# Kernel optimization log

Measured on AMD Instinct MI355X. Metric: run time of the kernel, lower is better.

## Reference

```python
import jax, jax.numpy as jnp
import numpy as np

SM_STEPS = 10

def setup_inputs() -> dict:
    key = jax.random.key(0)
    k0, k1, k2, k3 = jax.random.split(key, 4)
    B, N, D, A = 8, 2048, 512, 128
    X = jax.random.normal(k0, (B, N, D), jnp.float32)
    adj = jax.random.uniform(k1, (B, N, N), jnp.float32)
    adj = adj / jnp.sum(adj, axis=-1, keepdims=True)  # row-stochastic for stable diffusion
    mask = jnp.ones((B, N), jnp.float32)
    W1 = jax.random.normal(k2, (A, D), jnp.float32) / np.sqrt(D).astype(np.float32)
    b1 = jnp.zeros((A,), jnp.float32)
    w2 = jax.random.normal(k3, (1, A), jnp.float32) / np.sqrt(A).astype(np.float32)
    alpha_logit = jnp.zeros((), jnp.float32)  # trainable alpha = sigmoid(0) = 0.5
    return {"X": X, "adj": adj, "mask": mask, "W1": W1, "b1": b1, "w2": w2, "alpha_logit": alpha_logit}

def _sm(f, adj, alpha, num_steps):
    # approx Sm: g <- alpha * adj @ g + (1 - alpha) * f, iterated num_steps times
    def body(g, _):
        g = alpha * jnp.einsum('bij,bjd->bid', adj, g) + (1.0 - alpha) * f
        return g, None
    g, _ = jax.lax.scan(body, f, None, length=num_steps)
    return g

def reference(X, adj, mask, W1, b1, w2, alpha_logit):
    alpha = jax.nn.sigmoid(alpha_logit)
    Xs = _sm(X, adj, alpha, SM_STEPS)                     # sm_where == 'early'
    H = jnp.einsum('bnd,ad->bna', Xs, W1) + b1            # proj1: (B,N,att_dim)
    H = jax.nn.gelu(H, approximate=False)                 # torch gelu (erf)
    f = jnp.einsum('bna,oa->bno', H, w2)                  # proj2: (B,N,1)
    m = mask[..., None]                                   # (B,N,1)
    logits = jnp.where(m > 0, f, -jnp.inf)
    s = jax.nn.softmax(logits, axis=1)                    # masked softmax over bag dim
    z = jnp.einsum('bnd,bno->bd', Xs, s)                  # bmm(X^T, s).squeeze(-1)
    return z
```

## Files before the change

### kernel.cpp

```cpp
#include <hip/hip_runtime.h>

constexpr int BB = 8;
constexpr int NN = 2048;
constexpr int DD = 512;
constexpr int AA = 128;
constexpr int SM_STEPS = 10;

typedef __attribute__((ext_vector_type(8))) short bf16x8;
typedef __attribute__((ext_vector_type(4))) float f32x4;
typedef __attribute__((ext_vector_type(8))) unsigned short u16x8;

__device__ __forceinline__ float bf2f(unsigned short u) {
  unsigned int v = ((unsigned int)u) << 16;
  union { unsigned int i; float f; } c; c.i = v; return c.f;
}
__device__ __forceinline__ unsigned short f2bf(float f) {
  union { float f; unsigned int i; } c; c.f = f;
  unsigned int v = c.i;
  unsigned int r = (v + 0x7FFFu + ((v >> 16) & 1u)) >> 16;
  return (unsigned short)r;
}

#define GLOBAL_AS __attribute__((address_space(1)))
#define LDS_AS __attribute__((address_space(3)))

__device__ __forceinline__ void async16(const void* g, void* l) {
  __builtin_amdgcn_global_load_lds((GLOBAL_AS const void*)g, (LDS_AS void*)l, 16, 0, 0);
}

__global__ __launch_bounds__(256) void convert_adj_kernel(
    const float* __restrict__ adj, unsigned short* __restrict__ adjb) {
  size_t i = (size_t)blockIdx.x * blockDim.x + threadIdx.x;
  size_t total = (size_t)BB * NN * NN / 4;
  size_t stride = (size_t)gridDim.x * blockDim.x;
  for (; i < total; i += stride) {
    float4 v = ((const float4*)adj)[i];
    ushort4 o;
    o.x = f2bf(v.x); o.y = f2bf(v.y); o.z = f2bf(v.z); o.w = f2bf(v.w);
    ((ushort4*)adjb)[i] = o;
  }
}

__global__ __launch_bounds__(256) void convert_w1_kernel(
    const float* __restrict__ W1, unsigned short* __restrict__ w1b) {
  int i = blockIdx.x * 256 + threadIdx.x;
  float4 v = ((const float4*)W1)[i];
  ushort4 o;
  o.x = f2bf(v.x); o.y = f2bf(v.y); o.z = f2bf(v.z); o.w = f2bf(v.w);
  ((ushort4*)w1b)[i] = o;
}

__global__ __launch_bounds__(256) void transpose_x_kernel(
    const float* __restrict__ X, unsigned short* __restrict__ xt) {
  __shared__ float tile[64][65];
  const int b = blockIdx.z;
  const int n0 = blockIdx.x * 64, d0 = blockIdx.y * 64;
  const int t = threadIdx.x;
  for (int i = 0; i < 16; ++i) {
    int idx = t + i * 256;
    int r = idx >> 6, c = idx & 63;
    tile[r][c] = X[(size_t)b * NN * DD + (size_t)(n0 + r) * DD + d0 + c];
  }
  __syncthreads();
  for (int i = 0; i < 16; ++i) {
    int idx = t + i * 256;
    int r = idx >> 6, c = idx & 63;
    xt[(size_t)b * DD * NN + (size_t)(d0 + r) * NN + n0 + c] = f2bf(tile[c][r]);
  }
}

__global__ __launch_bounds__(256) void transpose_xs_kernel(
    const unsigned short* __restrict__ xst, unsigned short* __restrict__ gnorm) {
  __shared__ unsigned int tile[64][65];
  const int b = blockIdx.z;
  const int n0 = blockIdx.x * 64, d0 = blockIdx.y * 64;
  const int t = threadIdx.x;
  for (int i = 0; i < 16; ++i) {
    int idx = t + i * 256;
    int r = idx >> 6, c = idx & 63;
    tile[r][c] = xst[(size_t)b * DD * NN + (size_t)(d0 + r) * NN + n0 + c];
  }
  __syncthreads();
  for (int i = 0; i < 16; ++i) {
    int idx = t + i * 256;
    int r = idx >> 6, c = idx & 63;
    gnorm[(size_t)b * NN * DD + (size_t)(n0 + r) * DD + d0 + c] =
        (unsigned short)tile[c][r];
  }
}

__global__ __launch_bounds__(256) void sm_step_kernel(
    const unsigned short* __restrict__ adjb,
    const unsigned short* __restrict__ gin,
    const unsigned short* __restrict__ xt,
    unsigned short* __restrict__ gout,
    const float* __restrict__ alogit) {
  constexpr int BK = 64;
  __shared__ alignas(16) unsigned short As[128 * BK];
  __shared__ alignas(16) unsigned short Bs[128 * BK];

  const int t = threadIdx.x;
  const int b = blockIdx.z;
  const int m0 = blockIdx.y * 128;
  const int n0 = blockIdx.x * 128;

  const int lane = t & 63;
  const int wave = t >> 6;
  const int wr = wave >> 1, wc = wave & 1;
  const int ln = lane & 15, kq = lane >> 4;

  const unsigned short* gA =
      gin + (size_t)b * DD * NN + (size_t)(m0 + (t >> 3)) * NN + (t & 7) * 8;
  const unsigned short* gB =
      adjb + (size_t)b * NN * NN + (size_t)(n0 + (t >> 3)) * NN + (t & 7) * 8;

  f32x4 acc[4][4];
#pragma unroll
  for (int i = 0; i < 4; ++i)
#pragma unroll
    for (int j = 0; j < 4; ++j) acc[i][j] = {0.f, 0.f, 0.f, 0.f};

  for (int k0 = 0; k0 < NN; k0 += BK) {
#pragma unroll
    for (int c = 0; c < 4; ++c) {
      async16(gA + (size_t)(32 * c) * NN, As + 8 * t + 2048 * c);
      async16(gB + (size_t)(32 * c) * NN, Bs + 8 * t + 2048 * c);
    }
    gA += BK;
    gB += BK;
    asm volatile("s_waitcnt vmcnt(0)" ::: "memory");
    __syncthreads();

#pragma unroll
    for (int s = 0; s < 2; ++s) {
      bf16x8 af[4], bfr[4];
#pragma unroll
      for (int i = 0; i < 4; ++i)
        af[i] = *(const bf16x8*)(&As[(wr * 64 + i * 16 + ln) * BK + s * 32 + kq * 8]);
#pragma unroll
      for (int j = 0; j < 4; ++j)
        bfr[j] = *(const bf16x8*)(&Bs[(wc * 64 + j * 16 + ln) * BK + s * 32 + kq * 8]);
#pragma unroll
      for (int i = 0; i < 4; ++i)
#pragma unroll
        for (int j = 0; j < 4; ++j)
          acc[i][j] =
              __builtin_amdgcn_mfma_f32_16x16x32_bf16(af[i], bfr[j], acc[i][j], 0, 0, 0);
    }
    __syncthreads();
  }

  const float al = alogit[0];
  const float alpha = 1.0f / (1.0f + expf(-al));
  const float ia = 1.0f - alpha;

#pragma unroll
  for (int i = 0; i < 4; ++i) {
#pragma unroll
    for (int j = 0; j < 4; ++j) {
      const int mbase = m0 + wr * 64 + i * 16 + kq * 4;
      const int nn = n0 + wc * 64 + j * 16 + ln;
#pragma unroll
      for (int r = 0; r < 4; ++r) {
        size_t idx = (size_t)b * DD * NN + (size_t)(mbase + r) * NN + nn;
        float xv = bf2f(xt[idx]);
        gout[idx] = f2bf(alpha * acc[i][j][r] + ia * xv);
      }
    }
  }
}

__global__ __launch_bounds__(256) void proj_gemm_kernel(
    const unsigned short* __restrict__ gnorm,
    const unsigned short* __restrict__ w1b,
    const float* __restrict__ b1,
    const float* __restrict__ w2,
    float* __restrict__ fbuf) {
  constexpr int BK = 64;
  __shared__ alignas(16) unsigned short As[128 * BK];
  __shared__ alignas(16) unsigned short Bs[128 * BK];
  __shared__ float red[4][64];

  const int t = threadIdx.x;
  const int b = blockIdx.y;
  const int n0 = blockIdx.x * 128;

  const int lane = t & 63;
  const int wave = t >> 6;
  const int wr = wave >> 1, wc = wave & 1;
  const int ln = lane & 15, kq = lane >> 4;

  const unsigned short* gA =
      gnorm + (size_t)b * NN * DD + (size_t)(n0 + (t >> 3)) * DD + (t & 7) * 8;
  const unsigned short* gB = w1b + (size_t)(t >> 3) * DD + (t & 7) * 8;

  f32x4 acc[4][4];
#pragma unroll
  for (int i = 0; i < 4; ++i)
#pragma unroll
    for (int j = 0; j < 4; ++j) acc[i][j] = {0.f, 0.f, 0.f, 0.f};

  for (int k0 = 0; k0 < DD; k0 += BK) {
#pragma unroll
    for (int c = 0; c < 4; ++c) {
      async16(gA + (size_t)(32 * c) * DD, As + 8 * t + 2048 * c);
      async16(gB + (size_t)(32 * c) * DD, Bs + 8 * t + 2048 * c);
    }
    gA += BK;
    gB += BK;
    asm volatile("s_waitcnt vmcnt(0)" ::: "memory");
    __syncthreads();

#pragma unroll
    for (int s = 0; s < 2; ++s) {
      bf16x8 af[4], bfr[4];
#pragma unroll
      for (int i = 0; i < 4; ++i)
        af[i] = *(const bf16x8*)(&As[(wr * 64 + i * 16 + ln) * BK + s * 32 + kq * 8]);
#pragma unroll
      for (int j = 0; j < 4; ++j)
        bfr[j] = *(const bf16x8*)(&Bs[(wc * 64 + j * 16 + ln) * BK + s * 32 + kq * 8]);
#pragma unroll
      for (int i = 0; i < 4; ++i)
#pragma unroll
        for (int j = 0; j < 4; ++j)
          acc[i][j] =
              __builtin_amdgcn_mfma_f32_16x16x32_bf16(af[i], bfr[j], acc[i][j], 0, 0, 0);
    }
    __syncthreads();
  }

  float b1v[4], w2v[4];
#pragma unroll
  for (int j = 0; j < 4; ++j) {
    int a = wc * 64 + j * 16 + ln;
    b1v[j] = b1[a];
    w2v[j] = w2[a];
  }
  float p[4][4];
#pragma unroll
  for (int i = 0; i < 4; ++i)
#pragma unroll
    for (int r = 0; r < 4; ++r) {
      float s = 0.f;
#pragma unroll
      for (int j = 0; j < 4; ++j) {
        float x = acc[i][j][r] + b1v[j];
        float g = 0.5f * x * (1.0f + erff(x * 0.70710678118654752f));
        s += g * w2v[j];
      }
      p[i][r] = s;
    }
#pragma unroll
  for (int m = 1; m < 16; m <<= 1)
#pragma unroll
    for (int i = 0; i < 4; ++i)
#pragma unroll
      for (int r = 0; r < 4; ++r) p[i][r] += __shfl_xor(p[i][r], m);

  if (ln == 0) {
#pragma unroll
    for (int i = 0; i < 4; ++i)
#pragma unroll
      for (int r = 0; r < 4; ++r) red[wave][i * 16 + kq * 4 + r] = p[i][r];
  }
  __syncthreads();
  if (t < 128) {
    int w0 = (t >> 6) * 2, loc = t & 63;
    fbuf[(size_t)b * NN + n0 + t] = red[w0][loc] + red[w0 + 1][loc];
  }
}

__global__ __launch_bounds__(256) void softmax_kernel(
    const float* __restrict__ fbuf, const float* __restrict__ mask,
    float* __restrict__ sbuf) {
  __shared__ float red[8];
  const int b = blockIdx.x, t = threadIdx.x;
  float v[8];
  float mx = -INFINITY;
  for (int i = 0; i < 8; ++i) {
    int n = t + i * 256;
    float mk = mask[(size_t)b * NN + n];
    float lv = fbuf[(size_t)b * NN + n];
    v[i] = (mk > 0.f) ? lv : -INFINITY;
    mx = fmaxf(mx, v[i]);
  }
  for (int d = 32; d; d >>= 1) mx = fmaxf(mx, __shfl_xor(mx, d));
  if ((t & 63) == 0) red[t >> 6] = mx;
  __syncthreads();
  mx = fmaxf(fmaxf(red[0], red[1]), fmaxf(red[2], red[3]));
  float sum = 0.f;
  float e[8];
  for (int i = 0; i < 8; ++i) {
    e[i] = (v[i] == -INFINITY) ? 0.f : expf(v[i] - mx);
    sum += e[i];
  }
  for (int d = 32; d; d >>= 1) sum += __shfl_xor(sum, d);
  if ((t & 63) == 0) red[4 + (t >> 6)] = sum;
  __syncthreads();
  sum = red[4] + red[5] + red[6] + red[7];
  float inv = 1.0f / sum;
  for (int i = 0; i < 8; ++i) sbuf[(size_t)b * NN + t + i * 256] = e[i] * inv;
}

__global__ __launch_bounds__(256) void pool_kernel(
    const unsigned short* __restrict__ xst, const float* __restrict__ sbuf,
    float* __restrict__ zout) {
  __shared__ float sL[NN];
  const int b = blockIdx.y, t = threadIdx.x;
  const int d0 = blockIdx.x * 8;
  for (int i = 0; i < 8; ++i) sL[t + i * 256] = sbuf[(size_t)b * NN + t + i * 256];
  __syncthreads();
  const int row = t >> 5, c = t & 31;
  const int d = d0 + row;
  const unsigned short* xr = xst + (size_t)b * DD * NN + (size_t)d * NN;
  float acc = 0.f;
  for (int i = 0; i < 8; ++i) {
    int nb = c * 64 + i * 8;
    u16x8 x = *(const u16x8*)(xr + nb);
#pragma unroll
    for (int j = 0; j < 8; ++j) acc += bf2f((unsigned short)x[j]) * sL[nb + j];
  }
  for (int dlt = 16; dlt; dlt >>= 1) acc += __shfl_xor(acc, dlt);
  if (c == 0) zout[(size_t)b * DD + d] = acc;
}

extern "C" void kernel_launch(void* const* d_in, const int* in_sizes, int n_in,
                              void* d_out, int out_size, void* d_ws, size_t ws_size,
                              hipStream_t stream) {
  const float* X = (const float*)d_in[0];
  const float* adj = (const float*)d_in[1];
  const float* mask = (const float*)d_in[2];
  const float* W1 = (const float*)d_in[3];
  const float* b1 = (const float*)d_in[4];
  const float* w2 = (const float*)d_in[5];
  const float* alogit = (const float*)d_in[6];
  float* zout = (float*)d_out;

  char* ws = (char*)d_ws;
  unsigned short* adjb = (unsigned short*)ws;
  unsigned short* w1b = (unsigned short*)ws;
  unsigned short* xt = (unsigned short*)(ws + ((size_t)64 << 20));
  unsigned short* gnorm = (unsigned short*)(ws + ((size_t)64 << 20));
  unsigned short* p0 = (unsigned short*)(ws + ((size_t)80 << 20));
  unsigned short* p1 = (unsigned short*)(ws + ((size_t)96 << 20));
  float* fbuf = (float*)(ws + ((size_t)112 << 20));
  float* sbuf = (float*)(ws + ((size_t)112 << 20) + 65536);

  hipLaunchKernelGGL(convert_adj_kernel, dim3(2048), dim3(256), 0, stream, adj, adjb);
  hipLaunchKernelGGL(transpose_x_kernel, dim3(32, 8, 8), dim3(256), 0, stream, X, xt);

  const unsigned short* gin = xt;
  unsigned short* pp[2] = {p0, p1};
  for (int s = 0; s < SM_STEPS; ++s) {
    unsigned short* go = pp[s & 1];
    hipLaunchKernelGGL(sm_step_kernel, dim3(16, 4, 8), dim3(256), 0, stream, adjb, gin,
                       xt, go, alogit);
    gin = go;
  }

  hipLaunchKernelGGL(convert_w1_kernel, dim3(64), dim3(256), 0, stream, W1, w1b);
  hipLaunchKernelGGL(transpose_xs_kernel, dim3(32, 8, 8), dim3(256), 0, stream, gin,
                     gnorm);
  hipLaunchKernelGGL(proj_gemm_kernel, dim3(16, 8), dim3(256), 0, stream, gnorm, w1b,
                     b1, w2, fbuf);
  hipLaunchKernelGGL(softmax_kernel, dim3(8), dim3(256), 0, stream, fbuf, mask, sbuf);
  hipLaunchKernelGGL(pool_kernel, dim3(64, 8), dim3(256), 0, stream, gin, sbuf, zout);
}
```

Baseline: 587.6 us.

## Triple-buffer the diffusion GEMM with swizzled LDS and wider 128x256 tiles

The smoothing-step GEMM now loads tiles into a three-slot LDS ring buffer with async copies issued two K-steps ahead, replacing the old load-wait-compute loop that fully drained memory on every step. Each block grows to 512 threads covering a 128x256 output tile, which halves the grid and reuses each gin tile across more adj columns. LDS addresses are XOR-swizzled to avoid bank conflicts, and s_setprio is raised around the MFMA bursts. The cost is much more LDS per block (about 144 KB), which limits how many blocks fit per CU, and fewer blocks in total.

```diff
diff --git a/kernel.cpp b/kernel.cpp
--- a/kernel.cpp
+++ b/kernel.cpp
@@ -89,30 +89,58 @@
   }
 }
 
-__global__ __launch_bounds__(256) void sm_step_kernel(
+__global__ __launch_bounds__(512) void sm_step_kernel(
     const unsigned short* __restrict__ adjb,
     const unsigned short* __restrict__ gin,
     const unsigned short* __restrict__ xt,
     unsigned short* __restrict__ gout,
     const float* __restrict__ alogit) {
   constexpr int BK = 64;
-  __shared__ alignas(16) unsigned short As[128 * BK];
-  __shared__ alignas(16) unsigned short Bs[128 * BK];
+  __shared__ alignas(16) unsigned char Abuf[3][128 * BK * 2];
+  __shared__ alignas(16) unsigned char Bbuf[3][256 * BK * 2];
 
   const int t = threadIdx.x;
   const int b = blockIdx.z;
   const int m0 = blockIdx.y * 128;
-  const int n0 = blockIdx.x * 128;
+  const int n0 = blockIdx.x * 256;
 
   const int lane = t & 63;
   const int wave = t >> 6;
-  const int wr = wave >> 1, wc = wave & 1;
+  const int wr = wave >> 2;
+  const int wc = wave & 3;
   const int ln = lane & 15, kq = lane >> 4;
 
-  const unsigned short* gA =
-      gin + (size_t)b * DD * NN + (size_t)(m0 + (t >> 3)) * NN + (t & 7) * 8;
-  const unsigned short* gB =
-      adjb + (size_t)b * NN * NN + (size_t)(n0 + (t >> 3)) * NN + (t & 7) * 8;
+  const unsigned short* gA = gin + (size_t)b * DD * NN;
+  const unsigned short* gB = adjb + (size_t)b * NN * NN;
+  const unsigned short* aSrc[2];
+  const unsigned short* bSrc[4];
+  int aOff[2], bOff[4];
+#pragma unroll
+  for (int u = 0; u < 2; ++u) {
+    int o = u * 8192 + t * 16;
+    int q = o ^ (((o >> 7) & 7) << 4);
+    int row = q >> 7, colb = q & 127;
+    aSrc[u] = gA + (size_t)(m0 + row) * NN + colb / 2;
+    aOff[u] = o;
+  }
+#pragma unroll
+  for (int u = 0; u < 4; ++u) {
+    int o = u * 8192 + t * 16;
+    int q = o ^ (((o >> 7) & 7) << 4);
+    int row = q >> 7, colb = q & 127;
+    bSrc[u] = gB + (size_t)(n0 + row) * NN + colb / 2;
+    bOff[u] = o;
+  }
+
+#define STAGE(tkv)                                            \
+  do {                                                        \
+    const int sl_ = (tkv) % 3;                                \
+    const int kk_ = (tkv)*BK;                                 \
+    _Pragma("unroll") for (int u = 0; u < 2; ++u)             \
+        async16(aSrc[u] + kk_, &Abuf[sl_][aOff[u]]);          \
+    _Pragma("unroll") for (int u = 0; u < 4; ++u)             \
+        async16(bSrc[u] + kk_, &Bbuf[sl_][bOff[u]]);          \
+  } while (0)
 
   f32x4 acc[4][4];
 #pragma unroll
@@ -120,35 +148,55 @@
 #pragma unroll
     for (int j = 0; j < 4; ++j) acc[i][j] = {0.f, 0.f, 0.f, 0.f};
 
-  for (int k0 = 0; k0 < NN; k0 += BK) {
-#pragma unroll
-    for (int c = 0; c < 4; ++c) {
-      async16(gA + (size_t)(32 * c) * NN, As + 8 * t + 2048 * c);
-      async16(gB + (size_t)(32 * c) * NN, Bs + 8 * t + 2048 * c);
-    }
-    gA += BK;
-    gB += BK;
-    asm volatile("s_waitcnt vmcnt(0)" ::: "memory");
-    __syncthreads();
-
-#pragma unroll
-    for (int s = 0; s < 2; ++s) {
-      bf16x8 af[4], bfr[4];
-#pragma unroll
-      for (int i = 0; i < 4; ++i)
-        af[i] = *(const bf16x8*)(&As[(wr * 64 + i * 16 + ln) * BK + s * 32 + kq * 8]);
-#pragma unroll
-      for (int j = 0; j < 4; ++j)
-        bfr[j] = *(const bf16x8*)(&Bs[(wc * 64 + j * 16 + ln) * BK + s * 32 + kq * 8]);
-#pragma unroll
-      for (int i = 0; i < 4; ++i)
-#pragma unroll
-        for (int j = 0; j < 4; ++j)
-          acc[i][j] =
-              __builtin_amdgcn_mfma_f32_16x16x32_bf16(af[i], bfr[j], acc[i][j], 0, 0, 0);
-    }
-    __syncthreads();
-  }
+#define COMPUTE(slv)                                                          \
+  do {                                                                        \
+    const unsigned char* Ab_ = Abuf[(slv)];                                   \
+    const unsigned char* Bb_ = Bbuf[(slv)];                                   \
+    _Pragma("unroll") for (int qph = 0; qph < 4; ++qph) {                     \
+      const int qm_ = qph >> 1, qn_ = qph & 1;                                \
+      bf16x8 av_[2][2], bv_[2][2];                                            \
+      _Pragma("unroll") for (int ii = 0; ii < 2; ++ii)                        \
+          _Pragma("unroll") for (int ss = 0; ss < 2; ++ss) {                  \
+        int row_ = wr * 64 + (2 * qm_ + ii) * 16 + ln;                        \
+        int o_ = (row_ * 128 + ss * 64 + kq * 16) ^ ((row_ & 7) << 4);        \
+        av_[ii][ss] = *(const bf16x8*)(Ab_ + o_);                             \
+      }                                                                       \
+      _Pragma("unroll") for (int jj = 0; jj < 2; ++jj)                        \
+          _Pragma("unroll") for (int ss = 0; ss < 2; ++ss) {                  \
+        int row_ = wc * 64 + (2 * qn_ + jj) * 16 + ln;                        \
+        int o_ = (row_ * 128 + ss * 64 + kq * 16) ^ ((row_ & 7) << 4);        \
+        bv_[jj][ss] = *(const bf16x8*)(Bb_ + o_);                             \
+      }                                                                       \
+      __builtin_amdgcn_s_setprio(1);                                          \
+      _Pragma("unroll") for (int ii = 0; ii < 2; ++ii)                        \
+          _Pragma("unroll") for (int jj = 0; jj < 2; ++jj)                    \
+              _Pragma("unroll") for (int ss = 0; ss < 2; ++ss)                \
+                  acc[2 * qm_ + ii][2 * qn_ + jj] =                           \
+                      __builtin_amdgcn_mfma_f32_16x16x32_bf16(                \
+                          av_[ii][ss], bv_[jj][ss],                           \
+                          acc[2 * qm_ + ii][2 * qn_ + jj], 0, 0, 0);          \
+      __builtin_amdgcn_s_setprio(0);                                          \
+    }                                                                         \
+  } while (0)
+
+  STAGE(0);
+  STAGE(1);
+
+  for (int tk = 0; tk < 30; ++tk) {
+    asm volatile("s_waitcnt vmcnt(6)" ::: "memory");
+    __builtin_amdgcn_s_barrier();
+    STAGE(tk + 2);
+    COMPUTE(tk % 3);
+  }
+  asm volatile("s_waitcnt vmcnt(6)" ::: "memory");
+  __builtin_amdgcn_s_barrier();
+  COMPUTE(0);
+  asm volatile("s_waitcnt vmcnt(0)" ::: "memory");
+  __builtin_amdgcn_s_barrier();
+  COMPUTE(1);
+
+#undef STAGE
+#undef COMPUTE
 
   const float al = alogit[0];
   const float alpha = 1.0f / (1.0f + expf(-al));
@@ -354,7 +402,7 @@
   unsigned short* pp[2] = {p0, p1};
   for (int s = 0; s < SM_STEPS; ++s) {
     unsigned short* go = pp[s & 1];
-    hipLaunchKernelGGL(sm_step_kernel, dim3(16, 4, 8), dim3(256), 0, stream, adjb, gin,
+    hipLaunchKernelGGL(sm_step_kernel, dim3(8, 4, 8), dim3(512), 0, stream, adjb, gin,
                        xt, go, alogit);
     gin = go;
   }
```

Result: slower. 631.0 us (+7.4%).

## Triple-buffer sm_step GEMM with async loads and XOR-swizzled LDS layout

Applied to the files above, without the earlier changes.

The diffusion-step GEMM main loop moves from a single-buffered BK=64 tile, which waits for vmcnt(0) before every compute step, to a three-stage ring of BK=32 tiles. Global-to-LDS async copies for tile k+2 are issued before tile k is computed, so memory latency overlaps with the MFMA work. The LDS layout also gains an XOR swizzle to reduce bank conflicts on fragment reads, and the MFMA block is wrapped in setprio. The cost is one barrier per half-sized K step and a hard-coded trip count of 62 that assumes NN=2048.

```diff
diff --git a/kernel.cpp b/kernel.cpp
--- a/kernel.cpp
+++ b/kernel.cpp
@@ -95,9 +95,9 @@
     const unsigned short* __restrict__ xt,
     unsigned short* __restrict__ gout,
     const float* __restrict__ alogit) {
-  constexpr int BK = 64;
-  __shared__ alignas(16) unsigned short As[128 * BK];
-  __shared__ alignas(16) unsigned short Bs[128 * BK];
+  constexpr int BK = 32;
+  __shared__ alignas(16) unsigned char Abuf[3][128 * BK * 2];
+  __shared__ alignas(16) unsigned char Bbuf[3][128 * BK * 2];
 
   const int t = threadIdx.x;
   const int b = blockIdx.z;
@@ -106,13 +106,35 @@
 
   const int lane = t & 63;
   const int wave = t >> 6;
-  const int wr = wave >> 1, wc = wave & 1;
+  const int wr = wave >> 1;
+  const int wc = wave & 1;
   const int ln = lane & 15, kq = lane >> 4;
 
-  const unsigned short* gA =
-      gin + (size_t)b * DD * NN + (size_t)(m0 + (t >> 3)) * NN + (t & 7) * 8;
-  const unsigned short* gB =
-      adjb + (size_t)b * NN * NN + (size_t)(n0 + (t >> 3)) * NN + (t & 7) * 8;
+  const unsigned short* gA = gin + (size_t)b * DD * NN;
+  const unsigned short* gB = adjb + (size_t)b * NN * NN;
+  const unsigned short* aSrc[2];
+  const unsigned short* bSrc[2];
+  int ldsOff[2];
+#pragma unroll
+  for (int u = 0; u < 2; ++u) {
+    int o = u * 4096 + t * 16;
+    int q = o ^ (((o >> 7) & 7) << 4);
+    int row = 2 * (q >> 7) + ((q >> 6) & 1);
+    int kel = (q & 63) >> 1;
+    aSrc[u] = gA + (size_t)(m0 + row) * NN + kel;
+    bSrc[u] = gB + (size_t)(n0 + row) * NN + kel;
+    ldsOff[u] = o;
+  }
+
+#define STAGE(tkv)                                              \
+  do {                                                          \
+    const int sl_ = (tkv) % 3;                                  \
+    const int kk_ = (tkv)*BK;                                   \
+    async16(aSrc[0] + kk_, &Abuf[sl_][ldsOff[0]]);              \
+    async16(aSrc[1] + kk_, &Abuf[sl_][ldsOff[1]]);              \
+    async16(bSrc[0] + kk_, &Bbuf[sl_][ldsOff[0]]);              \
+    async16(bSrc[1] + kk_, &Bbuf[sl_][ldsOff[1]]);              \
+  } while (0)
 
   f32x4 acc[4][4];
 #pragma unroll
@@ -120,35 +142,51 @@
 #pragma unroll
     for (int j = 0; j < 4; ++j) acc[i][j] = {0.f, 0.f, 0.f, 0.f};
 
-  for (int k0 = 0; k0 < NN; k0 += BK) {
-#pragma unroll
-    for (int c = 0; c < 4; ++c) {
-      async16(gA + (size_t)(32 * c) * NN, As + 8 * t + 2048 * c);
-      async16(gB + (size_t)(32 * c) * NN, Bs + 8 * t + 2048 * c);
-    }
-    gA += BK;
-    gB += BK;
-    asm volatile("s_waitcnt vmcnt(0)" ::: "memory");
-    __syncthreads();
-
-#pragma unroll
-    for (int s = 0; s < 2; ++s) {
-      bf16x8 af[4], bfr[4];
-#pragma unroll
-      for (int i = 0; i < 4; ++i)
-        af[i] = *(const bf16x8*)(&As[(wr * 64 + i * 16 + ln) * BK + s * 32 + kq * 8]);
-#pragma unroll
-      for (int j = 0; j < 4; ++j)
-        bfr[j] = *(const bf16x8*)(&Bs[(wc * 64 + j * 16 + ln) * BK + s * 32 + kq * 8]);
-#pragma unroll
-      for (int i = 0; i < 4; ++i)
-#pragma unroll
-        for (int j = 0; j < 4; ++j)
-          acc[i][j] =
-              __builtin_amdgcn_mfma_f32_16x16x32_bf16(af[i], bfr[j], acc[i][j], 0, 0, 0);
-    }
-    __syncthreads();
-  }
+#define FRAG_OFF(row) \
+  ((((row) >> 1) * 128 + ((row)&1) * 64 + kq * 16) ^ ((((row) >> 1) & 7) << 4))
+
+#define COMPUTE(slv)                                                          \
+  do {                                                                        \
+    const unsigned char* Ab_ = Abuf[(slv)];                                   \
+    const unsigned char* Bb_ = Bbuf[(slv)];                                   \
+    bf16x8 av[4], bv[4];                                                      \
+    _Pragma("unroll") for (int ii = 0; ii < 4; ++ii) {                        \
+      int row_ = wr * 64 + ii * 16 + ln;                                      \
+      av[ii] = *(const bf16x8*)(Ab_ + FRAG_OFF(row_));                        \
+    }                                                                         \
+    _Pragma("unroll") for (int jj = 0; jj < 4; ++jj) {                        \
+      int row_ = wc * 64 + jj * 16 + ln;                                      \
+      bv[jj] = *(const bf16x8*)(Bb_ + FRAG_OFF(row_));                        \
+    }                                                                         \
+    asm volatile("s_waitcnt lgkmcnt(0)" ::: "memory");                        \
+    __builtin_amdgcn_sched_barrier(0);                                        \
+    __builtin_amdgcn_s_setprio(1);                                            \
+    _Pragma("unroll") for (int ii = 0; ii < 4; ++ii)                          \
+        _Pragma("unroll") for (int jj = 0; jj < 4; ++jj)                      \
+            acc[ii][jj] = __builtin_amdgcn_mfma_f32_16x16x32_bf16(            \
+                av[ii], bv[jj], acc[ii][jj], 0, 0, 0);                        \
+    __builtin_amdgcn_s_setprio(0);                                            \
+  } while (0)
+
+  STAGE(0);
+  STAGE(1);
+
+  for (int tk = 0; tk < 62; ++tk) {
+    asm volatile("s_waitcnt vmcnt(4)" ::: "memory");
+    __builtin_amdgcn_s_barrier();
+    STAGE(tk + 2);
+    COMPUTE(tk % 3);
+  }
+  asm volatile("s_waitcnt vmcnt(4)" ::: "memory");
+  __builtin_amdgcn_s_barrier();
+  COMPUTE(2);
+  asm volatile("s_waitcnt vmcnt(0)" ::: "memory");
+  __builtin_amdgcn_s_barrier();
+  COMPUTE(0);
+
+#undef COMPUTE
+#undef FRAG_OFF
+#undef STAGE
 
   const float al = alogit[0];
   const float alpha = 1.0f / (1.0f + expf(-al));
```

Result: slower. 692.1 us (+17.8%).
